# Optimization experiments

Measured on AMD Instinct MI355X. Metric: run time of the kernel, lower is better.

## Reference

```python
import jax, jax.numpy as jnp
import numpy as np

B, N_OBJS, HW = 2, 30, 64
W_H = HW * HW                      # 4096 visual tokens
N = W_H + 4 * N_OBJS + 64          # 4280 total tokens (satisfies the N - 4*n_objs - 64 == 64*64 check)
QUERY_DIM, HEADS, DIM_HEAD = 320, 8, 40
INNER = HEADS * DIM_HEAD


def setup_inputs() -> dict:
    key = jax.random.key(0)
    ks = jax.random.split(key, 7)
    x = jax.random.normal(ks[0], (B, N, QUERY_DIM), dtype=jnp.float32)
    # binary per-object instance masks on the 64x64 visual grid
    att_masks = (jax.random.uniform(ks[1], (B, N_OBJS, HW, HW)) < 0.15).astype(jnp.float32)
    s = 0.02
    Wq = jax.random.normal(ks[2], (QUERY_DIM, INNER), dtype=jnp.float32) * s
    Wk = jax.random.normal(ks[3], (QUERY_DIM, INNER), dtype=jnp.float32) * s
    Wv = jax.random.normal(ks[4], (QUERY_DIM, INNER), dtype=jnp.float32) * s
    Wo = jax.random.normal(ks[5], (INNER, QUERY_DIM), dtype=jnp.float32) * s
    bo = jax.random.normal(ks[6], (QUERY_DIM,), dtype=jnp.float32) * s
    return {"x": x, "att_masks": att_masks, "Wq": Wq, "Wk": Wk, "Wv": Wv, "Wo": Wo, "bo": bo}


def _build_mask(att_masks):
    # att_masks: [B, n_objs, 64, 64] -> additive/boolean grounding mask [B, 1, N, N]
    b, n_objs = att_masks.shape[0], att_masks.shape[1]
    m = att_masks.reshape(b, n_objs, W_H)                     # [B, O, 4096]
    # sum over objects of per-object outer products (bmm then sum over objs)
    ind = jnp.einsum('boi,boj->bij', m, m)                    # [B, 4096, 4096]
    # visual_token_masks ends up exactly 1 where ind>=1 else 0 (the two masked assigns)
    visual = (ind >= 1.0).astype(att_masks.dtype)
    mask = jnp.ones((b, 1, N, N), dtype=att_masks.dtype)
    mask = mask.at[:, :, :W_H, :W_H].set(visual[:, None])
    mr = m[:, None]                                           # [B, 1, O, 4096]
    rep_rows = jnp.tile(mr, (1, 1, 4, 1))                     # [B, 1, 4O, 4096]
    mask = mask.at[:, :, W_H:N - 64, :W_H].set(rep_rows)
    mask = mask.at[:, :, W_H + n_objs:W_H + 3 * n_objs, :W_H].set(1.0)
    rep_cols = jnp.tile(jnp.swapaxes(mr, 2, 3), (1, 1, 1, 4))  # [B, 1, 4096, 4O]
    mask = mask.at[:, :, :W_H, W_H:N - 64].set(rep_cols)
    mask = mask.at[:, :, :W_H, W_H + n_objs:W_H + 3 * n_objs].set(1.0)
    mask = mask + jnp.eye(N, dtype=att_masks.dtype)[None, None] * 1e-9
    return mask


def reference(x, att_masks, Wq, Wk, Wv, Wo, bo):
    b, n, _ = x.shape
    scale = DIM_HEAD ** -0.5
    q = (x @ Wq).reshape(b, n, HEADS, DIM_HEAD).transpose(0, 2, 1, 3)  # [B,H,N,C]
    k = (x @ Wk).reshape(b, n, HEADS, DIM_HEAD).transpose(0, 2, 1, 3)
    v = (x @ Wv).reshape(b, n, HEADS, DIM_HEAD).transpose(0, 2, 1, 3)
    mask = _build_mask(att_masks)                                      # [B,1,N,N]
    sim = jnp.einsum('bhic,bhjc->bhij', q, k) * scale                  # [B,H,N,N]
    sim = jnp.where(mask <= 0.0, -jnp.inf, sim)
    attn = jax.nn.softmax(sim, axis=-1)
    out = jnp.einsum('bhij,bhjc->bhic', attn, v)                       # [B,H,N,C]
    out = out.transpose(0, 2, 1, 3).reshape(b, n, INNER)
    return out @ Wo + bo
```

## Files before the change

### kernel.cpp

```cpp
#include <hip/hip_runtime.h>
#include <hip/hip_bf16.h>

#define BB 2
#define N_TOK 4280
#define NPAD 4352
#define MPAD 8576
#define WH 4096
#define NOBJ 30
#define QDIM 320
#define HEADS 8
#define DHEAD 40
#define M_ROWS (BB * N_TOK)
#define NT64 (NPAD / 64)
#define NQT (NPAD / 128)
#define KSPLIT 4
#define NTH (NT64 / KSPLIT)

typedef __attribute__((ext_vector_type(8))) short short8;
typedef __attribute__((ext_vector_type(4))) short short4v;
typedef __attribute__((ext_vector_type(4))) float f32x4;
typedef __attribute__((ext_vector_type(4))) unsigned uintx4;
typedef __attribute__((ext_vector_type(2))) unsigned long long u64x2;

#define GLD16(lds, g) __builtin_amdgcn_global_load_lds( \
    (const __attribute__((address_space(1))) unsigned*)(g), \
    (__attribute__((address_space(3))) unsigned*)(lds), 16, 0, 0)
#define GLD4(lds, g) __builtin_amdgcn_global_load_lds( \
    (const __attribute__((address_space(1))) unsigned*)(g), \
    (__attribute__((address_space(3))) unsigned*)(lds), 4, 0, 0)

__device__ __forceinline__ ushort f2bf(float x) {
    union { __hip_bfloat16 h; ushort u; } cv;
    cv.h = __float2bfloat16(x);
    return cv.u;
}
__device__ __forceinline__ float bf2f(ushort u) {
    union { unsigned u; float f; } cv;
    cv.u = ((unsigned)u) << 16;
    return cv.f;
}

__global__ void k_zero(u64x2* __restrict__ p, int n16) {
    int stride = gridDim.x * blockDim.x;
    u64x2 z = {0ull, 0ull};
    for (int i = blockIdx.x * blockDim.x + threadIdx.x; i < n16; i += stride)
        p[i] = z;
}

__global__ void k_bits(const float* __restrict__ att, unsigned* __restrict__ bits) {
    int gid = blockIdx.x * blockDim.x + threadIdx.x;
    if (gid >= BB * NPAD) return;
    int b = gid / NPAD, i = gid - b * NPAD;
    unsigned v = 0;
    if (i < WH) {
        const float* base = att + (size_t)b * NOBJ * WH + i;
        #pragma unroll
        for (int o = 0; o < NOBJ; ++o)
            if (base[(size_t)o * WH] > 0.5f) v |= (1u << o);
    }
    bits[gid] = v;
}

__global__ void k_xcvt(const float* __restrict__ x, ushort* __restrict__ xb) {
    int i = blockIdx.x * blockDim.x + threadIdx.x;
    if (i >= M_ROWS * QDIM / 8) return;
    float4 v0 = ((const float4*)x)[i * 2];
    float4 v1 = ((const float4*)x)[i * 2 + 1];
    short8 o;
    o[0] = (short)f2bf(v0.x); o[1] = (short)f2bf(v0.y);
    o[2] = (short)f2bf(v0.z); o[3] = (short)f2bf(v0.w);
    o[4] = (short)f2bf(v1.x); o[5] = (short)f2bf(v1.y);
    o[6] = (short)f2bf(v1.z); o[7] = (short)f2bf(v1.w);
    ((short8*)xb)[i] = o;
}

__global__ __launch_bounds__(256) void k_wcvt(const float* __restrict__ Wq,
                                              const float* __restrict__ Wk,
                                              const float* __restrict__ Wv,
                                              const float* __restrict__ Wo,
                                              ushort* __restrict__ WtAll) {
    __shared__ float T[32][33];
    const int k0 = blockIdx.x * 32;
    const int np0 = blockIdx.y * 32;
    const float SC = 0.15811388300841897f * 1.4426950408889634f;
    const float* src; int n0; float sc = 1.f;
    if (np0 < 320)      { src = Wq; n0 = np0;       sc = SC; }
    else if (np0 < 640) { src = Wk; n0 = np0 - 320; }
    else if (np0 < 960) { src = Wv; n0 = np0 - 640; }
    else                { src = Wo; n0 = np0 - 960; }
    const int tid = threadIdx.x;
    #pragma unroll
    for (int it = 0; it < 4; ++it) {
        int idx = tid + it * 256;
        int r = idx >> 5, c = idx & 31;
        T[r][c] = src[(size_t)(k0 + r) * QDIM + n0 + c];
    }
    __syncthreads();
    #pragma unroll
    for (int it = 0; it < 4; ++it) {
        int idx = tid + it * 256;
        int rr = idx >> 5, cc = idx & 31;
        WtAll[(size_t)(np0 + rr) * QDIM + k0 + cc] = f2bf(T[cc][rr] * sc);
    }
}

template<int IS_OUT>
__global__ __launch_bounds__(256) void k_mm(const ushort* __restrict__ A,
                                            const ushort* __restrict__ Wt,
                                            const float* __restrict__ bias,
                                            ushort* __restrict__ Qb,
                                            ushort* __restrict__ Kb,
                                            ushort* __restrict__ Vt,
                                            float* __restrict__ Cout) {
    __shared__ __align__(16) char Ab[2][8192];
    __shared__ __align__(16) char Bb[2][8192];
    const int tid = threadIdx.x, lane = tid & 63, wv = tid >> 6;
    const int g = lane >> 4, c16 = lane & 15, l7 = lane & 7;
    const int rsub = lane >> 3, slotx = lane & 7;
    const int m0 = blockIdx.x * 64;
    const int nt = blockIdx.y;

    f32x4 acc[4] = {{0,0,0,0},{0,0,0,0},{0,0,0,0},{0,0,0,0}};

    auto STAGE = [&](int ks, int bufi) {
        const int k0 = ks * 64;
        #pragma unroll
        for (int u = 0; u < 2; ++u) {
            int r0 = wv * 16 + u * 8;
            int row = r0 + rsub;
            int slot = slotx ^ (row & 7);
            GLD16(Ab[bufi] + r0 * 128, A + (size_t)(m0 + row) * QDIM + k0 + slot * 8);
            GLD16(Bb[bufi] + r0 * 128, Wt + (size_t)(nt * 64 + row) * QDIM + k0 + slot * 8);
        }
    };

    const int sl0 = (g ^ l7) * 16, sl1 = ((4 + g) ^ l7) * 16;

    STAGE(0, 0);
    __syncthreads();
    int cur = 0;
    for (int ks = 0; ks < 5; ++ks) {
        if (ks < 4) STAGE(ks + 1, cur ^ 1);
        const char* bbase = Bb[cur] + (wv * 16 + c16) * 128;
        short8 bf0 = *(const short8*)(bbase + sl0);
        short8 bf1 = *(const short8*)(bbase + sl1);
        #pragma unroll
        for (int mi = 0; mi < 4; ++mi) {
            const char* abase = Ab[cur] + (mi * 16 + c16) * 128;
            acc[mi] = __builtin_amdgcn_mfma_f32_16x16x32_bf16(*(const short8*)(abase + sl0), bf0, acc[mi], 0, 0, 0);
            acc[mi] = __builtin_amdgcn_mfma_f32_16x16x32_bf16(*(const short8*)(abase + sl1), bf1, acc[mi], 0, 0, 0);
        }
        __syncthreads();
        cur ^= 1;
    }

    const int ng = nt * 64 + wv * 16 + c16;
    if (IS_OUT) {
        float bv = bias[ng];
        #pragma unroll
        for (int mi = 0; mi < 4; ++mi)
            #pragma unroll
            for (int r = 0; r < 4; ++r) {
                int m = m0 + mi * 16 + g * 4 + r;
                if (m < M_ROWS) Cout[(size_t)m * QDIM + ng] = acc[mi][r] + bv;
            }
    } else {
        int p = ng / QDIM, nn = ng - p * QDIM;
        int h = nn / DHEAD, d = nn - h * DHEAD;
        if (p == 2) {
            #pragma unroll
            for (int mi = 0; mi < 4; ++mi) {
                int m = m0 + mi * 16 + g * 4;
                if (m >= M_ROWS) continue;
                int b = m / N_TOK, tok = m - b * N_TOK;
                short4v w4;
                w4[0] = (short)f2bf(acc[mi][0]);
                w4[1] = (short)f2bf(acc[mi][1]);
                w4[2] = (short)f2bf(acc[mi][2]);
                w4[3] = (short)f2bf(acc[mi][3]);
                *(short4v*)(Vt + ((size_t)(b * HEADS + h) * 48 + d) * NPAD + tok) = w4;
            }
        } else {
            ushort* base = (p == 0) ? Qb : Kb;
            #pragma unroll
            for (int mi = 0; mi < 4; ++mi)
                #pragma unroll
                for (int r = 0; r < 4; ++r) {
                    int m = m0 + mi * 16 + g * 4 + r;
                    if (m >= M_ROWS) continue;
                    int b = m / N_TOK, tok = m - b * N_TOK;
                    base[((size_t)(b * HEADS + h) * NPAD + tok) * 64 + d] = f2bf(acc[mi][r]);
                }
        }
    }
}

__global__ __launch_bounds__(256) void k_norm(const ushort* __restrict__ Qb,
                                              const ushort* __restrict__ Kb,
                                              float* __restrict__ Bsh) {
    __shared__ float rq[256], rk[256];
    const int bh = blockIdx.x, tid = threadIdx.x;
    float mq = 0.f, mk = 0.f;
    for (int tok = tid; tok < N_TOK; tok += 256) {
        const ushort* qp = Qb + ((size_t)bh * NPAD + tok) * 64;
        const ushort* kp = Kb + ((size_t)bh * NPAD + tok) * 64;
        float sq = 0.f, sk = 0.f;
        #pragma unroll
        for (int d8 = 0; d8 < 40; d8 += 8) {
            short8 a = *(const short8*)(qp + d8);
            short8 c = *(const short8*)(kp + d8);
            #pragma unroll
            for (int j = 0; j < 8; ++j) {
                float fa = bf2f((ushort)a[j]), fc = bf2f((ushort)c[j]);
                sq += fa * fa; sk += fc * fc;
            }
        }
        mq = fmaxf(mq, sq); mk = fmaxf(mk, sk);
    }
    rq[tid] = mq; rk[tid] = mk;
    __syncthreads();
    for (int s = 128; s > 0; s >>= 1) {
        if (tid < s) {
            rq[tid] = fmaxf(rq[tid], rq[tid + s]);
            rk[tid] = fmaxf(rk[tid], rk[tid + s]);
        }
        __syncthreads();
    }
    if (tid == 0) Bsh[bh] = sqrtf(rq[0]) * sqrtf(rk[0]);
}

__global__ void k_patch(ushort* __restrict__ Qb, ushort* __restrict__ Kb,
                        const float* __restrict__ Bsh) {
    int gid = blockIdx.x * blockDim.x + threadIdx.x;
    if (gid >= 16 * NPAD) return;
    int bh = gid / NPAD, tok = gid - bh * NPAD;
    float B = Bsh[bh];
    Qb[(size_t)gid * 64 + 40] = f2bf(-B);
    if (tok < N_TOK) Kb[(size_t)gid * 64 + 40] = (ushort)0x3F80;
}

__device__ __forceinline__ bool mask_ok(int i, int j, unsigned bi, unsigned bj) {
    if (j >= N_TOK) return false;
    if (i == j) return true;
    if (i < WH) {
        if (j < WH) return (bi & bj) != 0u;
        if (j >= WH + 4 * NOBJ) return true;
        int cI = j - WH;
        if ((unsigned)(cI - NOBJ) < (unsigned)(2 * NOBJ)) return true;
        int om = (cI < NOBJ) ? cI : cI - 3 * NOBJ;
        return ((bi >> om) & 1u) != 0u;
    }
    if (j >= WH) return true;
    if (i >= WH + 4 * NOBJ) return true;
    int rI = i - WH;
    if ((unsigned)(rI - NOBJ) < (unsigned)(2 * NOBJ)) return true;
    int om = (rI < NOBJ) ? rI : rI - 3 * NOBJ;
    return ((bj >> om) & 1u) != 0u;
}

__global__ __launch_bounds__(256, 4) void k_attn(const ushort* __restrict__ Qb,
                                                 const ushort* __restrict__ Kb,
                                                 const ushort* __restrict__ Vt,
                                                 const unsigned* __restrict__ bits,
                                                 float* __restrict__ Opart,
                                                 float* __restrict__ Lpart) {
    __shared__ __align__(16) char KtB[64 * 128];
    __shared__ __align__(16) char VtB[48 * 128];
    __shared__ __align__(16) char PsB[4 * 4096];
    __shared__ __align__(16) unsigned bJB[64];

    const int tid = threadIdx.x;
    const int lane = tid & 63, wv = tid >> 6;
    const int g = lane >> 4, c16 = lane & 15;
    const int l7x = c16 & 7;
    const int rsub = lane >> 3, slotx = lane & 7;

    const int bid = blockIdx.x;
    const int logical = (bid & 7) * 272 + (bid >> 3);
    const int grp = logical / NQT;
    const int qt = logical - grp * NQT;
    const int bh = grp >> 2, ks = grp & 3;
    const int b = bh >> 3;
    const int qb_blk = qt * 128;
    const int q0w = qb_blk + wv * 32;
    const int iqA = q0w + c16, iqB = iqA + 16;
    const bool vis_i = (qt < 32);
    const int t0 = ks * NTH;

    short8 qA0, qA1, qB0, qB1;
    {
        const ushort* qp = Qb + ((size_t)bh * NPAD + iqA) * 64 + g * 8;
        qA0 = *(const short8*)(qp);
        qA1 = *(const short8*)(qp + 32);
        qB0 = *(const short8*)(qp + 16 * 64);
        qB1 = *(const short8*)(qp + 16 * 64 + 32);
    }
    const unsigned bI_A = bits[(size_t)b * NPAD + iqA];
    const unsigned bI_B = bits[(size_t)b * NPAD + iqB];

    const ushort* kp = Kb + ((size_t)bh * NPAD + t0 * 64 + wv * 16 + rsub) * 64 + (slotx ^ rsub) * 8;
    const ushort* vbase = Vt + (size_t)bh * 48 * NPAD;
    int voff0 = 0, voff1 = 0;
    if (wv < 3) {
        int d0 = wv * 16 + rsub, d1 = d0 + 8;
        voff0 = d0 * NPAD + (slotx ^ rsub) * 8;
        voff1 = d1 * NPAD + (slotx ^ rsub) * 8;
    }
    const unsigned* bp = bits + (size_t)b * NPAD + t0 * 64 + lane;

    auto STAGE_K = [&](const ushort* kpt) {
        GLD16(KtB + (wv * 16) * 128, kpt);
        GLD16(KtB + (wv * 16 + 8) * 128, kpt + 512);
    };
    auto STAGE_V = [&](int j0) {
        if (wv < 3) {
            GLD16(VtB + (wv * 16) * 128, vbase + j0 + voff0);
            GLD16(VtB + (wv * 16 + 8) * 128, vbase + j0 + voff1);
        }
    };
    auto STAGE_B = [&](const unsigned* bpt) {
        if (wv == 3) GLD4(bJB, bpt);
    };

    const int sl0 = (g ^ l7x) * 16;
    const int sl1 = ((4 + g) ^ l7x) * 16;
    const int pswA = wv * 4096 + c16 * 128;
    const int pswB = pswA + 2048;
    const int swz = l7x << 4;

    float psA = 0.f, psB = 0.f;
    f32x4 oA0 = {0,0,0,0}, oA1 = oA0, oA2 = oA0;
    f32x4 oB0 = oA0, oB1 = oA0, oB2 = oA0;

    STAGE_K(kp); STAGE_V(t0 * 64); STAGE_B(bp);
    __syncthreads();

    for (int t = 0; t < NTH; ++t) {
        const int tg = t0 + t;
        const int j0 = tg * 64;

        auto do_tile = [&](auto okA_fn, auto okB_fn) {
            #pragma unroll
            for (int kt = 0; kt < 4; ++kt) {
                const char* arow = KtB + (kt * 16 + c16) * 128;
                short8 a0 = *(const short8*)(arow + sl0);
                short8 a1 = *(const short8*)(arow + sl1);
                f32x4 sA = {0,0,0,0}, sB = {0,0,0,0};
                __builtin_amdgcn_s_setprio(1);
                sA = __builtin_amdgcn_mfma_f32_16x16x32_bf16(a0, qA0, sA, 0, 0, 0);
                sA = __builtin_amdgcn_mfma_f32_16x16x32_bf16(a1, qA1, sA, 0, 0, 0);
                sB = __builtin_amdgcn_mfma_f32_16x16x32_bf16(a0, qB0, sB, 0, 0, 0);
                sB = __builtin_amdgcn_mfma_f32_16x16x32_bf16(a1, qB1, sB, 0, 0, 0);
                __builtin_amdgcn_s_setprio(0);
                uintx4 bk = *(const uintx4*)&bJB[kt * 16 + g * 4];
                float pA[4], pB[4];
                #pragma unroll
                for (int r = 0; r < 4; ++r) {
                    int j = j0 + kt * 16 + g * 4 + r;
                    float eA = __builtin_amdgcn_exp2f(sA[r]);
                    float eB = __builtin_amdgcn_exp2f(sB[r]);
                    pA[r] = okA_fn(j, bk[r]) ? eA : 0.f;
                    pB[r] = okB_fn(j, bk[r]) ? eB : 0.f;
                    psA += pA[r];
                    psB += pB[r];
                }
                unsigned wA0, wA1, wB0, wB1;
                asm("v_cvt_pk_bf16_f32 %0, %1, %2" : "=v"(wA0) : "v"(pA[0]), "v"(pA[1]));
                asm("v_cvt_pk_bf16_f32 %0, %1, %2" : "=v"(wA1) : "v"(pA[2]), "v"(pA[3]));
                asm("v_cvt_pk_bf16_f32 %0, %1, %2" : "=v"(wB0) : "v"(pB[0]), "v"(pB[1]));
                asm("v_cvt_pk_bf16_f32 %0, %1, %2" : "=v"(wB1) : "v"(pB[2]), "v"(pB[3]));
                uint2 vA; vA.x = wA0; vA.y = wA1;
                uint2 vB; vB.x = wB0; vB.y = wB1;
                int po = (kt * 32 + g * 8) ^ swz;
                *(uint2*)(PsB + pswA + po) = vA;
                *(uint2*)(PsB + pswB + po) = vB;
            }
        };

        const bool vis_j = (j0 + 64 <= WH);
        if (vis_i && vis_j && ((tg >> 1) != qt)) {
            do_tile([&](int j, unsigned bj) { return (bI_A & bj) != 0u; },
                    [&](int j, unsigned bj) { return (bI_B & bj) != 0u; });
        } else if (vis_i && vis_j) {
            do_tile([&](int j, unsigned bj) { return ((bI_A & bj) != 0u) || (iqA == j); },
                    [&](int j, unsigned bj) { return ((bI_B & bj) != 0u) || (iqB == j); });
        } else {
            do_tile([&](int j, unsigned bj) { return mask_ok(iqA, j, bI_A, bj); },
                    [&](int j, unsigned bj) { return mask_ok(iqB, j, bI_B, bj); });
        }

        __syncthreads();
        kp += 64 * 64; bp += 64;
        if (t + 1 < NTH) { STAGE_K(kp); STAGE_B(bp); }

        short8 paA0 = *(const short8*)(PsB + pswA + sl0);
        short8 paA1 = *(const short8*)(PsB + pswA + sl1);
        short8 paB0 = *(const short8*)(PsB + pswB + sl0);
        short8 paB1 = *(const short8*)(PsB + pswB + sl1);
        {
            const char* v0r = VtB + (0 * 16 + c16) * 128;
            const char* v1r = VtB + (1 * 16 + c16) * 128;
            const char* v2r = VtB + (2 * 16 + c16) * 128;
            short8 v00 = *(const short8*)(v0r + sl0), v01 = *(const short8*)(v0r + sl1);
            short8 v10 = *(const short8*)(v1r + sl0), v11 = *(const short8*)(v1r + sl1);
            short8 v20 = *(const short8*)(v2r + sl0), v21 = *(const short8*)(v2r + sl1);
            __builtin_amdgcn_s_setprio(1);
            oA0 = __builtin_amdgcn_mfma_f32_16x16x32_bf16(paA0, v00, oA0, 0, 0, 0);
            oA0 = __builtin_amdgcn_mfma_f32_16x16x32_bf16(paA1, v01, oA0, 0, 0, 0);
            oB0 = __builtin_amdgcn_mfma_f32_16x16x32_bf16(paB0, v00, oB0, 0, 0, 0);
            oB0 = __builtin_amdgcn_mfma_f32_16x16x32_bf16(paB1, v01, oB0, 0, 0, 0);
            oA1 = __builtin_amdgcn_mfma_f32_16x16x32_bf16(paA0, v10, oA1, 0, 0, 0);
            oA1 = __builtin_amdgcn_mfma_f32_16x16x32_bf16(paA1, v11, oA1, 0, 0, 0);
            oB1 = __builtin_amdgcn_mfma_f32_16x16x32_bf16(paB0, v10, oB1, 0, 0, 0);
            oB1 = __builtin_amdgcn_mfma_f32_16x16x32_bf16(paB1, v11, oB1, 0, 0, 0);
            oA2 = __builtin_amdgcn_mfma_f32_16x16x32_bf16(paA0, v20, oA2, 0, 0, 0);
            oA2 = __builtin_amdgcn_mfma_f32_16x16x32_bf16(paA1, v21, oA2, 0, 0, 0);
            oB2 = __builtin_amdgcn_mfma_f32_16x16x32_bf16(paB0, v20, oB2, 0, 0, 0);
            oB2 = __builtin_amdgcn_mfma_f32_16x16x32_bf16(paB1, v21, oB2, 0, 0, 0);
            __builtin_amdgcn_s_setprio(0);
        }

        __syncthreads();
        if (t + 1 < NTH) STAGE_V((tg + 1) * 64);
    }

    psA += __shfl_xor(psA, 16); psA += __shfl_xor(psA, 32);
    psB += __shfl_xor(psB, 16); psB += __shfl_xor(psB, 32);
    const size_t prow = ((size_t)ks * 16 + bh) * NPAD;
    if (g == 0) {
        Lpart[prow + q0w + c16]      = psA;
        Lpart[prow + q0w + 16 + c16] = psB;
    }
    #pragma unroll
    for (int r = 0; r < 4; ++r) {
        int qrA = q0w + g * 4 + r;
        int qrB = qrA + 16;
        if (qrA < N_TOK) {
            float* dst = Opart + (prow + qrA) * 40;
            dst[c16]      = oA0[r];
            dst[16 + c16] = oA1[r];
            if (c16 < 8) dst[32 + c16] = oA2[r];
        }
        if (qrB < N_TOK) {
            float* dst = Opart + (prow + qrB) * 40;
            dst[c16]      = oB0[r];
            dst[16 + c16] = oB1[r];
            if (c16 < 8) dst[32 + c16] = oB2[r];
        }
    }
}

__global__ __launch_bounds__(256) void k_comb(const float* __restrict__ Opart,
                                              const float* __restrict__ Lpart,
                                              ushort* __restrict__ AOb) {
    int gid = blockIdx.x * blockDim.x + threadIdx.x;
    if (gid >= 16 * N_TOK * 10) return;
    int row = gid / 10, v = gid - row * 10;
    int bh = row / N_TOK, q = row - bh * N_TOK;
    f32x4 s = {0.f, 0.f, 0.f, 0.f};
    float l = 0.f;
    #pragma unroll
    for (int ks = 0; ks < KSPLIT; ++ks) {
        size_t rr = ((size_t)ks * 16 + bh) * NPAD + q;
        f32x4 a = *(const f32x4*)(Opart + rr * 40 + v * 4);
        s[0] += a[0]; s[1] += a[1]; s[2] += a[2]; s[3] += a[3];
        l += Lpart[rr];
    }
    float inv = 1.f / l;
    int b = bh >> 3, h = bh & 7;
    short4v o;
    o[0] = (short)f2bf(s[0] * inv);
    o[1] = (short)f2bf(s[1] * inv);
    o[2] = (short)f2bf(s[2] * inv);
    o[3] = (short)f2bf(s[3] * inv);
    *(short4v*)(AOb + (size_t)(b * N_TOK + q) * QDIM + h * DHEAD + v * 4) = o;
}

extern "C" void kernel_launch(void* const* d_in, const int* in_sizes, int n_in,
                              void* d_out, int out_size, void* d_ws, size_t ws_size,
                              hipStream_t stream) {
    const float* x   = (const float*)d_in[0];
    const float* att = (const float*)d_in[1];
    const float* Wq  = (const float*)d_in[2];
    const float* Wk  = (const float*)d_in[3];
    const float* Wv  = (const float*)d_in[4];
    const float* Wo  = (const float*)d_in[5];
    const float* bo  = (const float*)d_in[6];
    float* out = (float*)d_out;

    char* w = (char*)d_ws;
    unsigned* bits = (unsigned*)w;
    float* Bsh = (float*)(w + 40960);
    size_t off = 65536;
    ushort* xb    = (ushort*)(w + off); off += (size_t)MPAD * QDIM * 2;
    ushort* WtAll = (ushort*)(w + off); off += (size_t)1280 * QDIM * 2;
    ushort* Qb    = (ushort*)(w + off); off += (size_t)16 * NPAD * 64 * 2;
    ushort* Kb    = (ushort*)(w + off); off += (size_t)16 * NPAD * 64 * 2;
    ushort* Vt    = (ushort*)(w + off); off += (size_t)16 * 48 * NPAD * 2;
    ushort* AOb   = (ushort*)(w + off); off += (size_t)MPAD * QDIM * 2;
    float*  Opart = (float*)(w + off);  off += (size_t)KSPLIT * 16 * NPAD * 40 * 4;
    float*  Lpart = (float*)(w + off);

    k_zero<<<2048, 256, 0, stream>>>((u64x2*)Qb, (int)((size_t)2 * 16 * NPAD * 64 * 2 / 16));
    k_bits<<<(BB * NPAD + 255) / 256, 256, 0, stream>>>(att, bits);
    k_xcvt<<<(M_ROWS * QDIM / 8 + 255) / 256, 256, 0, stream>>>(x, xb);
    k_wcvt<<<dim3(10, 40), 256, 0, stream>>>(Wq, Wk, Wv, Wo, WtAll);

    k_mm<0><<<dim3(MPAD / 64, 15), 256, 0, stream>>>(xb, WtAll, nullptr, Qb, Kb, Vt, nullptr);
    k_norm<<<16, 256, 0, stream>>>(Qb, Kb, Bsh);
    k_patch<<<(16 * NPAD + 255) / 256, 256, 0, stream>>>(Qb, Kb, Bsh);
    k_attn<<<16 * NQT * KSPLIT, 256, 0, stream>>>(Qb, Kb, Vt, bits, Opart, Lpart);
    k_comb<<<(16 * N_TOK * 10 + 255) / 256, 256, 0, stream>>>(Opart, Lpart, AOb);
    k_mm<1><<<dim3(MPAD / 64, 5), 256, 0, stream>>>(AOb, WtAll + 960 * QDIM, bo,
                                                    nullptr, nullptr, nullptr, out);
}
```

Measured before the change: 214.7 us.

## Double-buffer K/V/mask tiles and fold softmax row sums into PV MFMA

Adds second LDS buffers for K, V and mask bits so the next tile is prefetched while the current one is computed, removing one barrier per iteration. Writes a constant 1.0 row into the padded V channel 40 so the P·V MFMA yields the softmax denominator in the spare accumulator lane, replacing the per-element scalar sums and shuffle reduction. Uses more LDS per block, which may lower occupancy at the requested four blocks per CU. The row sum is now taken from bf16-rounded probabilities.

```diff
diff --git a/kernel.cpp b/kernel.cpp
--- a/kernel.cpp
+++ b/kernel.cpp
@@ -230,13 +230,14 @@
 }
 
 __global__ void k_patch(ushort* __restrict__ Qb, ushort* __restrict__ Kb,
-                        const float* __restrict__ Bsh) {
+                        ushort* __restrict__ Vt, const float* __restrict__ Bsh) {
     int gid = blockIdx.x * blockDim.x + threadIdx.x;
     if (gid >= 16 * NPAD) return;
     int bh = gid / NPAD, tok = gid - bh * NPAD;
     float B = Bsh[bh];
     Qb[(size_t)gid * 64 + 40] = f2bf(-B);
     if (tok < N_TOK) Kb[(size_t)gid * 64 + 40] = (ushort)0x3F80;
+    Vt[((size_t)bh * 48 + 40) * NPAD + tok] = (tok < N_TOK) ? (ushort)0x3F80 : (ushort)0;
 }
 
 __device__ __forceinline__ bool mask_ok(int i, int j, unsigned bi, unsigned bj) {
@@ -264,10 +265,10 @@
                                                  const unsigned* __restrict__ bits,
                                                  float* __restrict__ Opart,
                                                  float* __restrict__ Lpart) {
-    __shared__ __align__(16) char KtB[64 * 128];
-    __shared__ __align__(16) char VtB[48 * 128];
+    __shared__ __align__(16) char KtB[2][8192];
+    __shared__ __align__(16) char VtB[2][6144];
     __shared__ __align__(16) char PsB[4 * 4096];
-    __shared__ __align__(16) unsigned bJB[64];
+    __shared__ __align__(16) unsigned bJB[2][64];
 
     const int tid = threadIdx.x;
     const int lane = tid & 63, wv = tid >> 6;
@@ -308,18 +309,18 @@
     }
     const unsigned* bp = bits + (size_t)b * NPAD + t0 * 64 + lane;
 
-    auto STAGE_K = [&](const ushort* kpt) {
-        GLD16(KtB + (wv * 16) * 128, kpt);
-        GLD16(KtB + (wv * 16 + 8) * 128, kpt + 512);
+    auto STAGE_K = [&](const ushort* kpt, int bi) {
+        GLD16(KtB[bi] + (wv * 16) * 128, kpt);
+        GLD16(KtB[bi] + (wv * 16 + 8) * 128, kpt + 512);
     };
-    auto STAGE_V = [&](int j0) {
+    auto STAGE_V = [&](int j0, int bi) {
         if (wv < 3) {
-            GLD16(VtB + (wv * 16) * 128, vbase + j0 + voff0);
-            GLD16(VtB + (wv * 16 + 8) * 128, vbase + j0 + voff1);
+            GLD16(VtB[bi] + (wv * 16) * 128, vbase + j0 + voff0);
+            GLD16(VtB[bi] + (wv * 16 + 8) * 128, vbase + j0 + voff1);
         }
     };
-    auto STAGE_B = [&](const unsigned* bpt) {
-        if (wv == 3) GLD4(bJB, bpt);
+    auto STAGE_B = [&](const unsigned* bpt, int bi) {
+        if (wv == 3) GLD4(bJB[bi], bpt);
     };
 
     const int sl0 = (g ^ l7x) * 16;
@@ -328,21 +329,28 @@
     const int pswB = pswA + 2048;
     const int swz = l7x << 4;
 
-    float psA = 0.f, psB = 0.f;
     f32x4 oA0 = {0,0,0,0}, oA1 = oA0, oA2 = oA0;
     f32x4 oB0 = oA0, oB1 = oA0, oB2 = oA0;
 
-    STAGE_K(kp); STAGE_V(t0 * 64); STAGE_B(bp);
+    STAGE_K(kp, 0); STAGE_V(t0 * 64, 0); STAGE_B(bp, 0);
     __syncthreads();
+    int cur = 0;
 
     for (int t = 0; t < NTH; ++t) {
         const int tg = t0 + t;
         const int j0 = tg * 64;
 
+        kp += 64 * 64; bp += 64;
+        if (t + 1 < NTH) {
+            STAGE_K(kp, cur ^ 1);
+            STAGE_V((tg + 1) * 64, cur ^ 1);
+            STAGE_B(bp, cur ^ 1);
+        }
+
         auto do_tile = [&](auto okA_fn, auto okB_fn) {
             #pragma unroll
             for (int kt = 0; kt < 4; ++kt) {
-                const char* arow = KtB + (kt * 16 + c16) * 128;
+                const char* arow = KtB[cur] + (kt * 16 + c16) * 128;
                 short8 a0 = *(const short8*)(arow + sl0);
                 short8 a1 = *(const short8*)(arow + sl1);
                 f32x4 sA = {0,0,0,0}, sB = {0,0,0,0};
@@ -352,7 +360,7 @@
                 sB = __builtin_amdgcn_mfma_f32_16x16x32_bf16(a0, qB0, sB, 0, 0, 0);
                 sB = __builtin_amdgcn_mfma_f32_16x16x32_bf16(a1, qB1, sB, 0, 0, 0);
                 __builtin_amdgcn_s_setprio(0);
-                uintx4 bk = *(const uintx4*)&bJB[kt * 16 + g * 4];
+                uintx4 bk = *(const uintx4*)&bJB[cur][kt * 16 + g * 4];
                 float pA[4], pB[4];
                 #pragma unroll
                 for (int r = 0; r < 4; ++r) {
@@ -361,8 +369,6 @@
                     float eB = __builtin_amdgcn_exp2f(sB[r]);
                     pA[r] = okA_fn(j, bk[r]) ? eA : 0.f;
                     pB[r] = okB_fn(j, bk[r]) ? eB : 0.f;
-                    psA += pA[r];
-                    psB += pB[r];
                 }
                 unsigned wA0, wA1, wB0, wB1;
                 asm("v_cvt_pk_bf16_f32 %0, %1, %2" : "=v"(wA0) : "v"(pA[0]), "v"(pA[1]));
@@ -389,18 +395,14 @@
                     [&](int j, unsigned bj) { return mask_ok(iqB, j, bI_B, bj); });
         }
 
-        __syncthreads();
-        kp += 64 * 64; bp += 64;
-        if (t + 1 < NTH) { STAGE_K(kp); STAGE_B(bp); }
-
         short8 paA0 = *(const short8*)(PsB + pswA + sl0);
         short8 paA1 = *(const short8*)(PsB + pswA + sl1);
         short8 paB0 = *(const short8*)(PsB + pswB + sl0);
         short8 paB1 = *(const short8*)(PsB + pswB + sl1);
         {
-            const char* v0r = VtB + (0 * 16 + c16) * 128;
-            const char* v1r = VtB + (1 * 16 + c16) * 128;
-            const char* v2r = VtB + (2 * 16 + c16) * 128;
+            const char* v0r = VtB[cur] + (0 * 16 + c16) * 128;
+            const char* v1r = VtB[cur] + (1 * 16 + c16) * 128;
+            const char* v2r = VtB[cur] + (2 * 16 + c16) * 128;
             short8 v00 = *(const short8*)(v0r + sl0), v01 = *(const short8*)(v0r + sl1);
             short8 v10 = *(const short8*)(v1r + sl0), v11 = *(const short8*)(v1r + sl1);
             short8 v20 = *(const short8*)(v2r + sl0), v21 = *(const short8*)(v2r + sl1);
@@ -421,15 +423,16 @@
         }
 
         __syncthreads();
-        if (t + 1 < NTH) STAGE_V((tg + 1) * 64);
-    }
-
-    psA += __shfl_xor(psA, 16); psA += __shfl_xor(psA, 32);
-    psB += __shfl_xor(psB, 16); psB += __shfl_xor(psB, 32);
+        cur ^= 1;
+    }
+
     const size_t prow = ((size_t)ks * 16 + bh) * NPAD;
-    if (g == 0) {
-        Lpart[prow + q0w + c16]      = psA;
-        Lpart[prow + q0w + 16 + c16] = psB;
+    if (c16 == 8) {
+        #pragma unroll
+        for (int r = 0; r < 4; ++r) {
+            Lpart[prow + q0w + g * 4 + r]      = oA2[r];
+            Lpart[prow + q0w + 16 + g * 4 + r] = oB2[r];
+        }
     }
     #pragma unroll
     for (int r = 0; r < 4; ++r) {
@@ -508,7 +511,7 @@
 
     k_mm<0><<<dim3(MPAD / 64, 15), 256, 0, stream>>>(xb, WtAll, nullptr, Qb, Kb, Vt, nullptr);
     k_norm<<<16, 256, 0, stream>>>(Qb, Kb, Bsh);
-    k_patch<<<(16 * NPAD + 255) / 256, 256, 0, stream>>>(Qb, Kb, Bsh);
+    k_patch<<<(16 * NPAD + 255) / 256, 256, 0, stream>>>(Qb, Kb, Vt, Bsh);
     k_attn<<<16 * NQT * KSPLIT, 256, 0, stream>>>(Qb, Kb, Vt, bits, Opart, Lpart);
     k_comb<<<(16 * N_TOK * 10 + 255) / 256, 256, 0, stream>>>(Opart, Lpart, AOb);
     k_mm<1><<<dim3(MPAD / 64, 5), 256, 0, stream>>>(AOb, WtAll + 960 * QDIM, bo,
```

After: 226.7 us. +5.6%, slower.
